# Kernel optimization log

Measured on AMD Instinct MI355X. Metric: run time of the kernel, lower is better.

## Reference

```python
import jax, jax.numpy as jnp
import numpy as np

MLOG32 = float(np.log(32.0))


def _maxpool(x, k):
    # F.max_pool2d(stride=1, padding=k//2) pads with -inf, matching init value
    pad = k // 2
    return jax.lax.reduce_window(x, -jnp.inf, jax.lax.max, (1, 1, k, k), (1, 1, 1, 1),
                                 ((0, 0), (0, 0), (pad, pad), (pad, pad)))


def _minpool(x, k):
    return -_maxpool(-x, k)


def _local_sum(x, k):
    # conv2d with all-ones kxk kernel, zero padding, same spatial size
    pad = k // 2
    return jax.lax.reduce_window(x, 0.0, jax.lax.add, (1, 1, k, k), (1, 1, 1, 1),
                                 ((0, 0), (0, 0), (pad, pad), (pad, pad)))


def _conv3(x, kern):
    # torch conv2d == cross-correlation == lax conv (no kernel flip)
    return jax.lax.conv_general_dilated(x, kern, (1, 1), ((1, 1), (1, 1)),
                                        dimension_numbers=('NCHW', 'OIHW', 'NCHW'))


def _otsu(gray, bins=32):
    # vectorized per-batch Otsu threshold; gray in [0,1]
    B, _, H, W = gray.shape
    v = gray.reshape(B, -1)
    idx = jnp.clip((v * bins).astype(jnp.int32), 0, bins - 1)  # histc semantics, v==1 -> last bin
    hist = jax.vmap(lambda i: jnp.bincount(i, length=bins))(idx).astype(gray.dtype)
    p = hist / (H * W + 1e-6)
    xs = jnp.linspace(0.0, 1.0, bins, dtype=gray.dtype)
    omega = jnp.cumsum(p, axis=1)
    mu = jnp.cumsum(p * xs[None, :], axis=1)
    mu_t = mu[:, -1:]
    sigma_b2 = (mu_t * omega - mu) ** 2 / (omega * (1.0 - omega) + 1e-8)
    kbest = jnp.argmax(sigma_b2, axis=1)
    edges = jnp.linspace(0.0, 1.0, bins + 1, dtype=gray.dtype)
    return edges[kbest].reshape(B, 1, 1, 1)


def _concept_maps(image_rgb, cell_dilate=10, k_local=9):
    r, g, b = image_rgb[:, 0:1], image_rgb[:, 1:2], image_rgb[:, 2:3]
    gray = jnp.clip(0.5 * (0.299 * r + 0.587 * g + 0.114 * b + 1.0), 0.0, 1.0)
    thr = _otsu(gray)
    nuc = (gray <= thr).astype(gray.dtype)
    # morphological open+close, k=3
    e = _minpool(nuc, 3)
    d = _maxpool(e, 3)
    d = _maxpool(d, 3)
    e2 = _minpool(d, 3)
    nuc = (e2 > 0.5).astype(gray.dtype)
    er = _minpool(nuc, 3)
    boundary = jnp.maximum(nuc - er, 0.0)
    lap_k = jnp.array([[0, 1, 0], [1, -4, 1], [0, 1, 0]], dtype=gray.dtype).reshape(1, 1, 3, 3)
    lap = jnp.abs(_conv3(nuc, lap_k))
    den = _local_sum(boundary, 5) + 1e-6
    roughness = lap * boundary / den
    kx = jnp.array([[1, 0, -1], [2, 0, -2], [1, 0, -1]], dtype=gray.dtype).reshape(1, 1, 3, 3)
    ky = jnp.array([[1, 2, 1], [0, 0, 0], [-1, -2, -1]], dtype=gray.dtype).reshape(1, 1, 3, 3)
    gx = _conv3(gray, kx)
    gy = _conv3(gray, ky)
    ang = jnp.arctan2(gy, gx)
    den_orient = _local_sum(jnp.ones_like(gray), k_local) + 1e-6
    ms = _local_sum(jnp.sin(ang), k_local) / den_orient
    mc = _local_sum(jnp.cos(ang), k_local) / den_orient
    circ_var = 1.0 - jnp.sqrt(ms ** 2 + mc ** 2 + 1e-6)
    kd = cell_dilate if cell_dilate % 2 == 1 else cell_dilate + 1  # force odd
    cell = jnp.minimum(_maxpool(nuc, kd), 1.0)
    A_n = _local_sum(nuc, k_local)
    A_c = jnp.maximum(_local_sum(cell, k_local) - A_n, 1.0)
    nc = A_n / A_c
    g2 = _local_sum(gray * gray, k_local) / den_orient
    g1 = _local_sum(gray, k_local) / den_orient
    ent_like = jnp.log1p(jnp.maximum(g2 - g1 * g1, 0.0))
    z_maps = jnp.concatenate([roughness, circ_var, nc, ent_like], axis=1)
    return z_maps, nuc


def _energy_forward(image_rgb, cal_a, cal_b, alpha_logits, tau_p, Ht, Wt):
    z_maps, nuc = _concept_maps(image_rgb)
    z0 = jnp.log1p(jnp.maximum(z_maps[:, 0:1], 0.0))
    z1 = jnp.clip(z_maps[:, 1:2], 0.0, 1.0)
    z2 = jnp.log1p(jnp.maximum(z_maps[:, 2:3], 0.0))
    z3 = jnp.clip(z_maps[:, 3:4], 0.0, MLOG32)
    z_stable = jnp.concatenate([z0, z1, z2, z3], axis=1)
    z_cal = jax.nn.softplus(cal_a)[None, :, None, None] * z_stable + cal_b[None, :, None, None]
    alpha = jax.nn.softmax(alpha_logits)[None, :, None, None]
    E = jnp.sum(alpha * z_cal, axis=1, keepdims=True)
    B = E.shape[0]
    if (E.shape[2], E.shape[3]) != (Ht, Wt):
        E_t = jax.image.resize(E, (B, 1, Ht, Wt), method='linear')
    else:
        E_t = E
    tau = 0.2 + jax.nn.softplus(tau_p)
    A = jax.nn.softmax((-E_t / tau).reshape(B, 1, Ht * Wt), axis=-1).reshape(B, 1, Ht, Wt)
    return A, z_maps, nuc, E_t


def setup_inputs() -> dict:
    key = jax.random.key(0)
    k1, k2, k3, k4 = jax.random.split(key, 4)
    B, H, W = 16, 512, 512
    image_rgb = 2.0 * jax.random.uniform(k1, (B, 3, H, W), dtype=jnp.float32) - 1.0
    cal_a = 1.0 + 0.1 * jax.random.normal(k2, (4,), jnp.float32)
    cal_b = 0.1 * jax.random.normal(k3, (4,), jnp.float32)
    alpha_logits = 0.1 * jax.random.normal(k4, (4,), jnp.float32)
    tau_p = jnp.float32(0.5)
    return {"image_rgb": image_rgb, "cal_a": cal_a, "cal_b": cal_b,
            "alpha_logits": alpha_logits, "tau_p": tau_p, "target_h": 512, "target_w": 512}


def reference(image_rgb, cal_a, cal_b, alpha_logits, tau_p, target_h, target_w):
    return _energy_forward(image_rgb, cal_a, cal_b, alpha_logits, tau_p, int(target_h), int(target_w))
```

## Files before the change

### kernel.cpp

```cpp
#include <hip/hip_runtime.h>
#include <math.h>
#include <stdint.h>

#define HW 512
#define IMG (HW*HW)
#define MLOG32f 3.4657359027997265f

__device__ __forceinline__ float grayf(float r, float g, float b) {
    float t = __fadd_rn(__fadd_rn(__fmul_rn(0.299f, r), __fmul_rn(0.587f, g)), __fmul_rn(0.114f, b));
    float s = __fmul_rn(0.5f, __fadd_rn(t, 1.0f));
    return fminf(fmaxf(s, 0.0f), 1.0f);
}

__device__ __forceinline__ float softplusf(float x) {
    return fmaxf(x, 0.0f) + log1pf(expf(-fabsf(x)));
}

__device__ __forceinline__ uint64_t kmask(int lo, int hi) {
    return (1ull << hi) - (1ull << lo);
}

__global__ void k_init(const float* __restrict__ cal_a, const float* __restrict__ cal_b,
                       const float* __restrict__ alpha_logits, const float* __restrict__ tau_p,
                       int* __restrict__ hist, float* __restrict__ expsum,
                       float* __restrict__ sc, int B) {
    int tid = threadIdx.x;
    for (int i = tid; i < B * 32; i += blockDim.x) hist[i] = 0;
    for (int i = tid; i < B; i += blockDim.x) expsum[i] = 0.0f;
    if (tid == 0) {
        float al[4];
        float m = -1e30f;
        for (int c = 0; c < 4; c++) { al[c] = alpha_logits[c]; m = fmaxf(m, al[c]); }
        float e[4]; float s = 0.0f;
        for (int c = 0; c < 4; c++) { e[c] = expf(al[c] - m); s += e[c]; }
        float bias = 0.0f;
        for (int c = 0; c < 4; c++) {
            float alpha = e[c] / s;
            sc[c] = alpha * softplusf(cal_a[c]);
            bias += alpha * cal_b[c];
        }
        sc[4] = bias;
        sc[5] = 0.2f + softplusf(tau_p[0]);
    }
}

__global__ __launch_bounds__(256) void k_gray_hist(const float* __restrict__ img,
                                                   float* __restrict__ gray,
                                                   int* __restrict__ hist) {
    __shared__ int lh[32];
    int tid = threadIdx.x;
    int b = blockIdx.y;
    if (tid < 32) lh[tid] = 0;
    __syncthreads();
    const float4* rp = (const float4*)(img + (size_t)b * 3 * IMG);
    const float4* gp = (const float4*)(img + (size_t)b * 3 * IMG + IMG);
    const float4* bp = (const float4*)(img + (size_t)b * 3 * IMG + 2 * IMG);
    float4* op = (float4*)(gray + (size_t)b * IMG);
    int i = blockIdx.x * 256 + tid;
    float4 r = rp[i], g = gp[i], bb = bp[i];
    float4 o;
    o.x = grayf(r.x, g.x, bb.x);
    o.y = grayf(r.y, g.y, bb.y);
    o.z = grayf(r.z, g.z, bb.z);
    o.w = grayf(r.w, g.w, bb.w);
    op[i] = o;
    int b0 = min(max((int)(o.x * 32.0f), 0), 31);
    int b1 = min(max((int)(o.y * 32.0f), 0), 31);
    int b2 = min(max((int)(o.z * 32.0f), 0), 31);
    int b3 = min(max((int)(o.w * 32.0f), 0), 31);
    atomicAdd(&lh[b0], 1); atomicAdd(&lh[b1], 1);
    atomicAdd(&lh[b2], 1); atomicAdd(&lh[b3], 1);
    __syncthreads();
    if (tid < 32) atomicAdd(&hist[b * 32 + tid], lh[tid]);
}

__global__ void k_otsu(const int* __restrict__ hist, float* __restrict__ thr, int B) {
    int b = threadIdx.x;
    if (b >= B) return;
    const int* h = hist + b * 32;
    float omega[32], mu[32];
    float co = 0.0f, cm = 0.0f;
    for (int k = 0; k < 32; k++) {
        float pk = (float)h[k] * (1.0f / 262144.0f);
        float xs = (float)((double)k / 31.0);
        co += pk;
        cm += pk * xs;
        omega[k] = co; mu[k] = cm;
    }
    float mu_t = mu[31];
    float best = -1e30f; int kb = 0;
    for (int k = 0; k < 32; k++) {
        float t = mu_t * omega[k] - mu[k];
        float sb = (t * t) / (omega[k] * (1.0f - omega[k]) + 1e-8f);
        if (sb > best) { best = sb; kb = k; }
    }
    thr[b] = (float)kb * 0.03125f;
}

__global__ __launch_bounds__(256) void k_thresh(const float* __restrict__ gray,
                                                const float* __restrict__ thr,
                                                uint32_t* __restrict__ packed) {
    int b = blockIdx.y;
    int i = blockIdx.x * 256 + threadIdx.x;
    float t = thr[b];
    float v = gray[(size_t)b * IMG + i];
    unsigned long long m = __ballot(v <= t);
    if ((threadIdx.x & 63) == 0)
        *(uint64_t*)&packed[(size_t)b * 8192 + (i >> 5)] = m;
}

__global__ __launch_bounds__(256) void k_morph(const uint32_t* __restrict__ p0,
                                               float* __restrict__ nuc,
                                               uint32_t* __restrict__ pn) {
    __shared__ uint64_t s0[40], s1[40];
    int tid = threadIdx.x, b = blockIdx.z;
    int x0 = blockIdx.x * 32, y0 = blockIdx.y * 32;
    int w0 = x0 >> 5;
    const uint32_t* pb = p0 + (size_t)b * 8192;
    int xlo = (x0 == 0) ? 4 : 0;
    int xhi = (x0 == 480) ? 36 : 40;
    uint64_t mwin = kmask(xlo, xhi);

    if (tid < 40) {
        int y = y0 - 4 + tid;
        uint64_t v = 0;
        if ((unsigned)y < (unsigned)HW) {
            const uint32_t* rowp = pb + y * 16;
            uint64_t wm = (w0 > 0)  ? rowp[w0 - 1] : 0;
            uint64_t wc = rowp[w0];
            uint64_t wp = (w0 < 15) ? rowp[w0 + 1] : 0;
            v = ((wm >> 28) | (wc << 4) | (wp << 36)) & kmask(0, 40);
        }
        s0[tid] = v;
    }
    __syncthreads();
    if (tid >= 1 && tid < 39) {
        uint64_t e = ~0ull;
        for (int dq = -1; dq <= 1; dq++) {
            int q = tid + dq;
            int y = y0 - 4 + q;
            uint64_t m = ((unsigned)y < (unsigned)HW) ? mwin : 0;
            uint64_t v = s0[q] | ~m;
            e &= v & (v << 1) & (v >> 1);
        }
        s1[tid] = e;
    }
    __syncthreads();
    if (tid >= 2 && tid < 38) {
        uint64_t d = 0;
        uint64_t me = kmask(1, 39);
        for (int dq = -1; dq <= 1; dq++) {
            int q = tid + dq;
            int y = y0 - 4 + q;
            uint64_t m = ((unsigned)y < (unsigned)HW) ? (mwin & me) : 0;
            uint64_t v = s1[q] & m;
            d |= v | (v << 1) | (v >> 1);
        }
        s0[tid] = d;
    }
    __syncthreads();
    if (tid >= 3 && tid < 37) {
        uint64_t d = 0;
        uint64_t me = kmask(2, 38);
        for (int dq = -1; dq <= 1; dq++) {
            int q = tid + dq;
            int y = y0 - 4 + q;
            uint64_t m = ((unsigned)y < (unsigned)HW) ? (mwin & me) : 0;
            uint64_t v = s0[q] & m;
            d |= v | (v << 1) | (v >> 1);
        }
        s1[tid] = d;
    }
    __syncthreads();
    if (tid >= 4 && tid < 36) {
        uint64_t e = ~0ull;
        uint64_t me = kmask(3, 37);
        for (int dq = -1; dq <= 1; dq++) {
            int q = tid + dq;
            int y = y0 - 4 + q;
            uint64_t m = ((unsigned)y < (unsigned)HW) ? (mwin & me) : 0;
            uint64_t v = s1[q] | ~m;
            e &= v & (v << 1) & (v >> 1);
        }
        s0[tid] = e;
    }
    __syncthreads();
    if (tid < 32) {
        int y = y0 + tid;
        pn[(size_t)b * 8192 + y * 16 + w0] = (uint32_t)(s0[tid + 4] >> 4);
    }
    float* nb = nuc + (size_t)b * IMG;
    for (int k = 0; k < 4; k++) {
        int i = tid + k * 256;
        int py = i >> 5, px = i & 31;
        nb[(size_t)(y0 + py) * HW + x0 + px] = (float)((s0[py + 4] >> (px + 4)) & 1);
    }
}

__global__ __launch_bounds__(256) void k_gray_maps(const float* __restrict__ gray,
                                                   float* zmap) {
    __shared__ float gt[42 * 43];
    __shared__ float st[40 * 41];
    __shared__ float ct[40 * 41];
    __shared__ float rs0[40 * 33];
    __shared__ float rs1[40 * 33];
    int tid = threadIdx.x, b = blockIdx.z;
    int x0 = blockIdx.x * 32, y0 = blockIdx.y * 32;
    const float* gb = gray + (size_t)b * IMG;
    for (int i = tid; i < 42 * 42; i += 256) {
        int ly = i / 42, lx = i % 42;
        int gy = y0 + ly - 5, gx = x0 + lx - 5;
        gt[ly * 43 + lx] = (gy >= 0 && gy < HW && gx >= 0 && gx < HW) ? gb[gy * HW + gx] : 0.0f;
    }
    __syncthreads();
    for (int i = tid; i < 1600; i += 256) {
        int ly = i / 40, lx = i % 40;
        int gy = y0 + ly - 4, gx = x0 + lx - 4;
        float s = 0.0f, c = 0.0f;
        if (gy >= 0 && gy < HW && gx >= 0 && gx < HW) {
            float a00 = gt[ly * 43 + lx],       a01 = gt[ly * 43 + lx + 1],       a02 = gt[ly * 43 + lx + 2];
            float a10 = gt[(ly + 1) * 43 + lx],                                   a12 = gt[(ly + 1) * 43 + lx + 2];
            float a20 = gt[(ly + 2) * 43 + lx], a21 = gt[(ly + 2) * 43 + lx + 1], a22 = gt[(ly + 2) * 43 + lx + 2];
            float gxv = (a00 - a02) + 2.0f * (a10 - a12) + (a20 - a22);
            float gyv = (a00 + 2.0f * a01 + a02) - (a20 + 2.0f * a21 + a22);
            float r2 = gxv * gxv + gyv * gyv;
            if (r2 > 0.0f) { float r = sqrtf(r2); s = gyv / r; c = gxv / r; }
            else { s = 0.0f; c = 1.0f; }
        }
        st[ly * 41 + lx] = s; ct[ly * 41 + lx] = c;
    }
    __syncthreads();
    for (int i = tid; i < 40 * 32; i += 256) {
        int ly = i / 32, lx = i % 32;
        float ss = 0.0f, cs = 0.0f;
        for (int dx = 0; dx < 9; dx++) { ss += st[ly * 41 + lx + dx]; cs += ct[ly * 41 + lx + dx]; }
        rs0[ly * 33 + lx] = ss; rs1[ly * 33 + lx] = cs;
    }
    __syncthreads();
    float z1v[4];
    for (int k = 0; k < 4; k++) {
        int j = tid + k * 256; int py = j >> 5, px = j & 31;
        float ss = 0.0f, cs = 0.0f;
        for (int dy = 0; dy < 9; dy++) { ss += rs0[(py + dy) * 33 + px]; cs += rs1[(py + dy) * 33 + px]; }
        int gy = y0 + py, gx = x0 + px;
        float cnty = (float)(min(gy + 4, HW - 1) - max(gy - 4, 0) + 1);
        float cntx = (float)(min(gx + 4, HW - 1) - max(gx - 4, 0) + 1);
        float den = cnty * cntx + 1e-6f;
        float ms = ss / den, mc = cs / den;
        z1v[k] = 1.0f - sqrtf(ms * ms + mc * mc + 1e-6f);
    }
    __syncthreads();
    for (int i = tid; i < 40 * 32; i += 256) {
        int ly = i / 32, lx = i % 32;
        float gs = 0.0f, g2s = 0.0f;
        for (int dx = 1; dx <= 9; dx++) { float v = gt[(ly + 1) * 43 + lx + dx]; gs += v; g2s += v * v; }
        rs0[ly * 33 + lx] = gs; rs1[ly * 33 + lx] = g2s;
    }
    __syncthreads();
    float* z1p = zmap + ((size_t)b * 4 + 1) * IMG;
    float* z3p = zmap + ((size_t)b * 4 + 3) * IMG;
    for (int k = 0; k < 4; k++) {
        int j = tid + k * 256; int py = j >> 5, px = j & 31;
        float gs = 0.0f, g2s = 0.0f;
        for (int dy = 0; dy < 9; dy++) { gs += rs0[(py + dy) * 33 + px]; g2s += rs1[(py + dy) * 33 + px]; }
        int gy = y0 + py, gx = x0 + px;
        float cnty = (float)(min(gy + 4, HW - 1) - max(gy - 4, 0) + 1);
        float cntx = (float)(min(gx + 4, HW - 1) - max(gx - 4, 0) + 1);
        float den = cnty * cntx + 1e-6f;
        float g1 = gs / den, g2 = g2s / den;
        z1p[gy * HW + gx] = z1v[k];
        z3p[gy * HW + gx] = log1pf(fmaxf(g2 - g1 * g1, 0.0f));
    }
}

__global__ __launch_bounds__(256) void k_nuc_maps(const uint32_t* __restrict__ pn,
                                                  float* zmap,
                                                  float* __restrict__ Eout,
                                                  const float* __restrict__ sc,
                                                  float* __restrict__ expsum) {
    __shared__ uint64_t nrow[50];
    __shared__ uint64_t ehr[50];
    __shared__ uint64_t dilh[50];
    __shared__ uint64_t bnd[36];
    __shared__ uint64_t cell[40];
    __shared__ int rs_n[40][32];
    __shared__ int rs_c[40][32];
    __shared__ int rs_b[36][32];
    __shared__ float red[256];
    int tid = threadIdx.x, b = blockIdx.z;
    int x0 = blockIdx.x * 32, y0 = blockIdx.y * 32;
    int w0 = x0 >> 5;
    const uint32_t* pb = pn + (size_t)b * 8192;
    int xlo = (x0 == 0) ? 9 : 0;
    int xhi = (x0 == 480) ? 41 : 50;
    uint64_t mwin = kmask(xlo, xhi);

    if (tid < 50) {
        int y = y0 - 9 + tid;
        uint64_t v = 0;
        if ((unsigned)y < (unsigned)HW) {
            const uint32_t* rowp = pb + y * 16;
            uint64_t wm = (w0 > 0)  ? rowp[w0 - 1] : 0;
            uint64_t wc = rowp[w0];
            uint64_t wp = (w0 < 15) ? rowp[w0 + 1] : 0;
            v = ((wm >> 23) | (wc << 9) | (wp << 41)) & kmask(0, 50);
        }
        nrow[tid] = v;
    }
    __syncthreads();
    if (tid < 50) {
        uint64_t v = nrow[tid];
        uint64_t d = v | (v << 1) | (v >> 1);
        d = d | (d << 2) | (d >> 2);
        d = d | (d << 2) | (d >> 2);
        dilh[tid] = d;
    }
    if (tid >= 6 && tid < 44) {
        int y = y0 - 9 + tid;
        uint64_t m = ((unsigned)y < (unsigned)HW) ? mwin : 0;
        uint64_t v = nrow[tid] | ~m;
        ehr[tid] = v & (v << 1) & (v >> 1);
    }
    __syncthreads();
    if (tid < 36) {
        int r = tid + 7;
        uint64_t er = ehr[r - 1] & ehr[r] & ehr[r + 1];
        bnd[tid] = nrow[r] & ~er;
    }
    if (tid < 40) {
        int r = tid + 5;
        int y = y0 - 4 + tid;
        uint64_t c = 0;
        for (int d = -5; d <= 5; d++) c |= dilh[r + d];
        uint64_t m = ((unsigned)y < (unsigned)HW) ? mwin : 0;
        cell[tid] = c & m;
    }
    __syncthreads();
    for (int i = tid; i < 40 * 32; i += 256) {
        int rr = i >> 5, p = i & 31;
        rs_n[rr][p] = __popcll((nrow[rr + 5] >> (p + 5)) & 0x1FFull);
        rs_c[rr][p] = __popcll((cell[rr]     >> (p + 5)) & 0x1FFull);
    }
    for (int i = tid; i < 36 * 32; i += 256) {
        int rr = i >> 5, p = i & 31;
        rs_b[rr][p] = __popcll((bnd[rr] >> (p + 7)) & 0x1Full);
    }
    __syncthreads();
    if (tid < 96) {
        int p = tid & 31, a = tid >> 5;
        if (a == 0)      { int s = 0; for (int rr = 0; rr < 40; rr++) { s += rs_n[rr][p]; rs_n[rr][p] = s; } }
        else if (a == 1) { int s = 0; for (int rr = 0; rr < 40; rr++) { s += rs_c[rr][p]; rs_c[rr][p] = s; } }
        else             { int s = 0; for (int rr = 0; rr < 36; rr++) { s += rs_b[rr][p]; rs_b[rr][p] = s; } }
    }
    __syncthreads();

    float w0f = sc[0], w1f = sc[1], w2f = sc[2], w3f = sc[3], bias = sc[4], tau = sc[5];
    const float* z1p = zmap + ((size_t)b * 4 + 1) * IMG;
    const float* z3p = zmap + ((size_t)b * 4 + 3) * IMG;
    float* z0p = zmap + ((size_t)b * 4 + 0) * IMG;
    float* z2p = zmap + ((size_t)b * 4 + 2) * IMG;
    float* Ep = Eout + (size_t)b * IMG;
    float acc = 0.0f;
    for (int k = 0; k < 4; k++) {
        int j = tid + k * 256; int py = j >> 5, p = j & 31;
        int An = rs_n[py + 8][p] - (py ? rs_n[py - 1][p] : 0);
        int Ac = rs_c[py + 8][p] - (py ? rs_c[py - 1][p] : 0);
        int db = rs_b[py + 4][p] - (py ? rs_b[py - 1][p] : 0);
        int r = py + 9, kk = p + 9;
        uint64_t rowc = nrow[r];
        int c   = (int)((rowc >> kk) & 1);
        int nb4 = (int)((nrow[r - 1] >> kk) & 1) + (int)((nrow[r + 1] >> kk) & 1)
                + (int)((rowc >> (kk - 1)) & 1) + (int)((rowc >> (kk + 1)) & 1);
        int lap = nb4 - 4 * c; lap = lap < 0 ? -lap : lap;
        int bc  = (int)((bnd[py + 2] >> kk) & 1);
        float den = (float)db + 1e-6f;
        float rough = (float)(lap * bc) / den;
        float z2 = (float)An / fmaxf((float)(Ac - An), 1.0f);
        int gy = y0 + py, gx = x0 + p;
        float z1 = z1p[gy * HW + gx], z3 = z3p[gy * HW + gx];
        float z0s = log1pf(fmaxf(rough, 0.0f));
        float z1s = fminf(fmaxf(z1, 0.0f), 1.0f);
        float z2s = log1pf(fmaxf(z2, 0.0f));
        float z3s = fminf(fmaxf(z3, 0.0f), MLOG32f);
        float E = w0f * z0s + w1f * z1s + w2f * z2s + w3f * z3s + bias;
        z0p[gy * HW + gx] = rough;
        z2p[gy * HW + gx] = z2;
        Ep[gy * HW + gx] = E;
        acc += expf(-E / tau);
    }
    red[tid] = acc;
    __syncthreads();
    for (int s = 128; s > 0; s >>= 1) {
        if (tid < s) red[tid] += red[tid + s];
        __syncthreads();
    }
    if (tid == 0) atomicAdd(&expsum[b], red[0]);
}

__global__ __launch_bounds__(256) void k_softmaxA(const float* __restrict__ E,
                                                  float* __restrict__ A,
                                                  const float* __restrict__ sc,
                                                  const float* __restrict__ expsum) {
    int b = blockIdx.y;
    int i = blockIdx.x * 256 + threadIdx.x;
    float tau = sc[5], S = expsum[b];
    const float4* Ep = (const float4*)(E + (size_t)b * IMG);
    float4* Ap = (float4*)(A + (size_t)b * IMG);
    float4 e = Ep[i];
    float4 o;
    o.x = expf(-e.x / tau) / S;
    o.y = expf(-e.y / tau) / S;
    o.z = expf(-e.z / tau) / S;
    o.w = expf(-e.w / tau) / S;
    Ap[i] = o;
}

extern "C" void kernel_launch(void* const* d_in, const int* in_sizes, int n_in,
                              void* d_out, int out_size, void* d_ws, size_t ws_size,
                              hipStream_t stream) {
    const float* img   = (const float*)d_in[0];
    const float* cal_a = (const float*)d_in[1];
    const float* cal_b = (const float*)d_in[2];
    const float* alpha = (const float*)d_in[3];
    const float* tau_p = (const float*)d_in[4];
    int B = in_sizes[0] / (3 * IMG);

    float* out  = (float*)d_out;
    float* A    = out;
    float* zmap = out + (size_t)B * IMG;
    float* nuc  = out + (size_t)B * IMG * 5;
    float* E    = out + (size_t)B * IMG * 6;
    float* gray = A;

    int*      hist    = (int*)d_ws;
    float*    thr     = (float*)d_ws + B * 32;
    float*    sc      = thr + B;
    float*    expsum  = sc + 8;
    uint32_t* packed0 = (uint32_t*)d_ws + 1024;
    uint32_t* packedN = packed0 + (size_t)B * 8192;

    k_init<<<1, 256, 0, stream>>>(cal_a, cal_b, alpha, tau_p, hist, expsum, sc, B);
    k_gray_hist<<<dim3(IMG / 1024, B), 256, 0, stream>>>(img, gray, hist);
    k_otsu<<<1, 64, 0, stream>>>(hist, thr, B);
    k_thresh<<<dim3(IMG / 256, B), 256, 0, stream>>>(gray, thr, packed0);
    dim3 tg(HW / 32, HW / 32, B);
    k_morph<<<tg, 256, 0, stream>>>(packed0, nuc, packedN);
    k_gray_maps<<<tg, 256, 0, stream>>>(gray, zmap);
    k_nuc_maps<<<tg, 256, 0, stream>>>(packedN, zmap, E, sc, expsum);
    k_softmaxA<<<dim3(IMG / 1024, B), 256, 0, stream>>>(E, A, sc, expsum);
}
```

Measured before the change: 287.6 us.

## Fuse gray-map and nucleus-map kernels, move nuc write, use fast math intrinsics

Merges k_gray_maps and k_nuc_maps into one k_maps kernel. The z1/z3 values stay in registers instead of being written to global memory and read back, and shared memory is aliased between the two phases. The float nuc map is now written from k_maps instead of k_morph. Divisions, sqrt, log1p and exp are replaced with hardware rcp/rsq/__logf/__expf, and the block reduction switches to wavefront shuffles. This trades some numerical precision for fewer instructions and less memory traffic.

Result: faster. 257.5 us (-10.5%).

```diff
diff --git a/kernel.cpp b/kernel.cpp
--- a/kernel.cpp
+++ b/kernel.cpp
@@ -15,6 +15,10 @@
 __device__ __forceinline__ float softplusf(float x) {
     return fmaxf(x, 0.0f) + log1pf(expf(-fabsf(x)));
 }
+
+__device__ __forceinline__ float frcp(float x)  { return __builtin_amdgcn_rcpf(x); }
+__device__ __forceinline__ float frsq(float x)  { return __builtin_amdgcn_rsqf(x); }
+__device__ __forceinline__ float flog1p(float x){ return __logf(1.0f + x); }
 
 __device__ __forceinline__ uint64_t kmask(int lo, int hi) {
     return (1ull << hi) - (1ull << lo);
@@ -40,7 +44,9 @@
             bias += alpha * cal_b[c];
         }
         sc[4] = bias;
-        sc[5] = 0.2f + softplusf(tau_p[0]);
+        float tau = 0.2f + softplusf(tau_p[0]);
+        sc[5] = tau;
+        sc[6] = -1.0f / tau;
     }
 }
 
@@ -110,7 +116,6 @@
 }
 
 __global__ __launch_bounds__(256) void k_morph(const uint32_t* __restrict__ p0,
-                                               float* __restrict__ nuc,
                                                uint32_t* __restrict__ pn) {
     __shared__ uint64_t s0[40], s1[40];
     int tid = threadIdx.x, b = blockIdx.z;
@@ -189,30 +194,68 @@
         int y = y0 + tid;
         pn[(size_t)b * 8192 + y * 16 + w0] = (uint32_t)(s0[tid + 4] >> 4);
     }
-    float* nb = nuc + (size_t)b * IMG;
-    for (int k = 0; k < 4; k++) {
-        int i = tid + k * 256;
-        int py = i >> 5, px = i & 31;
-        nb[(size_t)(y0 + py) * HW + x0 + px] = (float)((s0[py + 4] >> (px + 4)) & 1);
-    }
-}
-
-__global__ __launch_bounds__(256) void k_gray_maps(const float* __restrict__ gray,
-                                                   float* zmap) {
-    __shared__ float gt[42 * 43];
-    __shared__ float st[40 * 41];
-    __shared__ float ct[40 * 41];
-    __shared__ float rs0[40 * 33];
-    __shared__ float rs1[40 * 33];
+}
+
+__global__ __launch_bounds__(256) void k_maps(const float* __restrict__ gray,
+                                              const uint32_t* __restrict__ pn,
+                                              float* __restrict__ zmap,
+                                              float* __restrict__ nucf,
+                                              float* __restrict__ Eout,
+                                              const float* __restrict__ sc,
+                                              float* __restrict__ expsum) {
+    __shared__ __align__(16) char smem[30912];
+    __shared__ uint64_t nrow[50], ehr[50], dilh[50], bnd[36], cell[40];
+    __shared__ float red[4];
+    float* gt  = (float*)smem;
+    float* st  = (float*)(smem + 7232);
+    float* ct  = (float*)(smem + 13792);
+    float* rs0 = (float*)(smem + 20352);
+    float* rs1 = (float*)(smem + 25632);
+    int* rs_n = (int*)smem;
+    int* rs_c = (int*)(smem + 5120);
+    int* rs_b = (int*)(smem + 10240);
+
     int tid = threadIdx.x, b = blockIdx.z;
     int x0 = blockIdx.x * 32, y0 = blockIdx.y * 32;
+    int w0 = x0 >> 5;
     const float* gb = gray + (size_t)b * IMG;
+    const uint32_t* pb = pn + (size_t)b * 8192;
+    int xlo = (x0 == 0) ? 9 : 0;
+    int xhi = (x0 == 480) ? 41 : 50;
+    uint64_t mwin = kmask(xlo, xhi);
+
     for (int i = tid; i < 42 * 42; i += 256) {
         int ly = i / 42, lx = i % 42;
         int gy = y0 + ly - 5, gx = x0 + lx - 5;
         gt[ly * 43 + lx] = (gy >= 0 && gy < HW && gx >= 0 && gx < HW) ? gb[gy * HW + gx] : 0.0f;
     }
-    __syncthreads();
+    if (tid < 50) {
+        int y = y0 - 9 + tid;
+        uint64_t v = 0;
+        if ((unsigned)y < (unsigned)HW) {
+            const uint32_t* rowp = pb + y * 16;
+            uint64_t wm = (w0 > 0)  ? rowp[w0 - 1] : 0;
+            uint64_t wc = rowp[w0];
+            uint64_t wp = (w0 < 15) ? rowp[w0 + 1] : 0;
+            v = ((wm >> 23) | (wc << 9) | (wp << 41)) & kmask(0, 50);
+        }
+        nrow[tid] = v;
+    }
+    __syncthreads();
+
+    if (tid < 50) {
+        uint64_t v = nrow[tid];
+        uint64_t d = v | (v << 1) | (v >> 1);
+        d = d | (d << 2) | (d >> 2);
+        d = d | (d << 2) | (d >> 2);
+        dilh[tid] = d;
+    }
+    if (tid >= 6 && tid < 44) {
+        int y = y0 - 9 + tid;
+        uint64_t m = ((unsigned)y < (unsigned)HW) ? mwin : 0;
+        uint64_t v = nrow[tid] | ~m;
+        ehr[tid] = v & (v << 1) & (v >> 1);
+    }
     for (int i = tid; i < 1600; i += 256) {
         int ly = i / 40, lx = i % 40;
         int gy = y0 + ly - 4, gx = x0 + lx - 4;
@@ -224,19 +267,34 @@
             float gxv = (a00 - a02) + 2.0f * (a10 - a12) + (a20 - a22);
             float gyv = (a00 + 2.0f * a01 + a02) - (a20 + 2.0f * a21 + a22);
             float r2 = gxv * gxv + gyv * gyv;
-            if (r2 > 0.0f) { float r = sqrtf(r2); s = gyv / r; c = gxv / r; }
+            if (r2 > 0.0f) { float ir = frsq(r2); s = gyv * ir; c = gxv * ir; }
             else { s = 0.0f; c = 1.0f; }
         }
         st[ly * 41 + lx] = s; ct[ly * 41 + lx] = c;
     }
     __syncthreads();
+
+    if (tid < 36) {
+        int r = tid + 7;
+        uint64_t er = ehr[r - 1] & ehr[r] & ehr[r + 1];
+        bnd[tid] = nrow[r] & ~er;
+    }
+    if (tid < 40) {
+        int r = tid + 5;
+        int y = y0 - 4 + tid;
+        uint64_t c = 0;
+        for (int d = -5; d <= 5; d++) c |= dilh[r + d];
+        uint64_t m = ((unsigned)y < (unsigned)HW) ? mwin : 0;
+        cell[tid] = c & m;
+    }
     for (int i = tid; i < 40 * 32; i += 256) {
-        int ly = i / 32, lx = i % 32;
+        int ly = i >> 5, lx = i & 31;
         float ss = 0.0f, cs = 0.0f;
         for (int dx = 0; dx < 9; dx++) { ss += st[ly * 41 + lx + dx]; cs += ct[ly * 41 + lx + dx]; }
         rs0[ly * 33 + lx] = ss; rs1[ly * 33 + lx] = cs;
     }
     __syncthreads();
+
     float z1v[4];
     for (int k = 0; k < 4; k++) {
         int j = tid + k * 256; int py = j >> 5, px = j & 31;
@@ -245,20 +303,19 @@
         int gy = y0 + py, gx = x0 + px;
         float cnty = (float)(min(gy + 4, HW - 1) - max(gy - 4, 0) + 1);
         float cntx = (float)(min(gx + 4, HW - 1) - max(gx - 4, 0) + 1);
-        float den = cnty * cntx + 1e-6f;
-        float ms = ss / den, mc = cs / den;
+        float iden = frcp(cnty * cntx + 1e-6f);
+        float ms = ss * iden, mc = cs * iden;
         z1v[k] = 1.0f - sqrtf(ms * ms + mc * mc + 1e-6f);
     }
     __syncthreads();
     for (int i = tid; i < 40 * 32; i += 256) {
-        int ly = i / 32, lx = i % 32;
+        int ly = i >> 5, lx = i & 31;
         float gs = 0.0f, g2s = 0.0f;
         for (int dx = 1; dx <= 9; dx++) { float v = gt[(ly + 1) * 43 + lx + dx]; gs += v; g2s += v * v; }
         rs0[ly * 33 + lx] = gs; rs1[ly * 33 + lx] = g2s;
     }
     __syncthreads();
-    float* z1p = zmap + ((size_t)b * 4 + 1) * IMG;
-    float* z3p = zmap + ((size_t)b * 4 + 3) * IMG;
+    float z3v[4];
     for (int k = 0; k < 4; k++) {
         int j = tid + k * 256; int py = j >> 5, px = j & 31;
         float gs = 0.0f, g2s = 0.0f;
@@ -266,135 +323,71 @@
         int gy = y0 + py, gx = x0 + px;
         float cnty = (float)(min(gy + 4, HW - 1) - max(gy - 4, 0) + 1);
         float cntx = (float)(min(gx + 4, HW - 1) - max(gx - 4, 0) + 1);
-        float den = cnty * cntx + 1e-6f;
-        float g1 = gs / den, g2 = g2s / den;
-        z1p[gy * HW + gx] = z1v[k];
-        z3p[gy * HW + gx] = log1pf(fmaxf(g2 - g1 * g1, 0.0f));
-    }
-}
-
-__global__ __launch_bounds__(256) void k_nuc_maps(const uint32_t* __restrict__ pn,
-                                                  float* zmap,
-                                                  float* __restrict__ Eout,
-                                                  const float* __restrict__ sc,
-                                                  float* __restrict__ expsum) {
-    __shared__ uint64_t nrow[50];
-    __shared__ uint64_t ehr[50];
-    __shared__ uint64_t dilh[50];
-    __shared__ uint64_t bnd[36];
-    __shared__ uint64_t cell[40];
-    __shared__ int rs_n[40][32];
-    __shared__ int rs_c[40][32];
-    __shared__ int rs_b[36][32];
-    __shared__ float red[256];
-    int tid = threadIdx.x, b = blockIdx.z;
-    int x0 = blockIdx.x * 32, y0 = blockIdx.y * 32;
-    int w0 = x0 >> 5;
-    const uint32_t* pb = pn + (size_t)b * 8192;
-    int xlo = (x0 == 0) ? 9 : 0;
-    int xhi = (x0 == 480) ? 41 : 50;
-    uint64_t mwin = kmask(xlo, xhi);
-
-    if (tid < 50) {
-        int y = y0 - 9 + tid;
-        uint64_t v = 0;
-        if ((unsigned)y < (unsigned)HW) {
-            const uint32_t* rowp = pb + y * 16;
-            uint64_t wm = (w0 > 0)  ? rowp[w0 - 1] : 0;
-            uint64_t wc = rowp[w0];
-            uint64_t wp = (w0 < 15) ? rowp[w0 + 1] : 0;
-            v = ((wm >> 23) | (wc << 9) | (wp << 41)) & kmask(0, 50);
-        }
-        nrow[tid] = v;
-    }
-    __syncthreads();
-    if (tid < 50) {
-        uint64_t v = nrow[tid];
-        uint64_t d = v | (v << 1) | (v >> 1);
-        d = d | (d << 2) | (d >> 2);
-        d = d | (d << 2) | (d >> 2);
-        dilh[tid] = d;
-    }
-    if (tid >= 6 && tid < 44) {
-        int y = y0 - 9 + tid;
-        uint64_t m = ((unsigned)y < (unsigned)HW) ? mwin : 0;
-        uint64_t v = nrow[tid] | ~m;
-        ehr[tid] = v & (v << 1) & (v >> 1);
-    }
-    __syncthreads();
-    if (tid < 36) {
-        int r = tid + 7;
-        uint64_t er = ehr[r - 1] & ehr[r] & ehr[r + 1];
-        bnd[tid] = nrow[r] & ~er;
-    }
-    if (tid < 40) {
-        int r = tid + 5;
-        int y = y0 - 4 + tid;
-        uint64_t c = 0;
-        for (int d = -5; d <= 5; d++) c |= dilh[r + d];
-        uint64_t m = ((unsigned)y < (unsigned)HW) ? mwin : 0;
-        cell[tid] = c & m;
-    }
-    __syncthreads();
+        float iden = frcp(cnty * cntx + 1e-6f);
+        float g1 = gs * iden, g2 = g2s * iden;
+        z3v[k] = flog1p(fmaxf(g2 - g1 * g1, 0.0f));
+    }
+    __syncthreads();
+
     for (int i = tid; i < 40 * 32; i += 256) {
         int rr = i >> 5, p = i & 31;
-        rs_n[rr][p] = __popcll((nrow[rr + 5] >> (p + 5)) & 0x1FFull);
-        rs_c[rr][p] = __popcll((cell[rr]     >> (p + 5)) & 0x1FFull);
+        rs_n[rr * 32 + p] = __popcll((nrow[rr + 5] >> (p + 5)) & 0x1FFull);
+        rs_c[rr * 32 + p] = __popcll((cell[rr]     >> (p + 5)) & 0x1FFull);
     }
     for (int i = tid; i < 36 * 32; i += 256) {
         int rr = i >> 5, p = i & 31;
-        rs_b[rr][p] = __popcll((bnd[rr] >> (p + 7)) & 0x1Full);
+        rs_b[rr * 32 + p] = __popcll((bnd[rr] >> (p + 7)) & 0x1Full);
     }
     __syncthreads();
     if (tid < 96) {
         int p = tid & 31, a = tid >> 5;
-        if (a == 0)      { int s = 0; for (int rr = 0; rr < 40; rr++) { s += rs_n[rr][p]; rs_n[rr][p] = s; } }
-        else if (a == 1) { int s = 0; for (int rr = 0; rr < 40; rr++) { s += rs_c[rr][p]; rs_c[rr][p] = s; } }
-        else             { int s = 0; for (int rr = 0; rr < 36; rr++) { s += rs_b[rr][p]; rs_b[rr][p] = s; } }
-    }
-    __syncthreads();
-
-    float w0f = sc[0], w1f = sc[1], w2f = sc[2], w3f = sc[3], bias = sc[4], tau = sc[5];
-    const float* z1p = zmap + ((size_t)b * 4 + 1) * IMG;
-    const float* z3p = zmap + ((size_t)b * 4 + 3) * IMG;
+        if (a == 0)      { int s = 0; for (int rr = 0; rr < 40; rr++) { s += rs_n[rr * 32 + p]; rs_n[rr * 32 + p] = s; } }
+        else if (a == 1) { int s = 0; for (int rr = 0; rr < 40; rr++) { s += rs_c[rr * 32 + p]; rs_c[rr * 32 + p] = s; } }
+        else             { int s = 0; for (int rr = 0; rr < 36; rr++) { s += rs_b[rr * 32 + p]; rs_b[rr * 32 + p] = s; } }
+    }
+    __syncthreads();
+
+    float w0f = sc[0], w1f = sc[1], w2f = sc[2], w3f = sc[3], bias = sc[4], ntau = sc[6];
     float* z0p = zmap + ((size_t)b * 4 + 0) * IMG;
+    float* z1p = zmap + ((size_t)b * 4 + 1) * IMG;
     float* z2p = zmap + ((size_t)b * 4 + 2) * IMG;
-    float* Ep = Eout + (size_t)b * IMG;
+    float* z3p = zmap + ((size_t)b * 4 + 3) * IMG;
+    float* Ep  = Eout + (size_t)b * IMG;
+    float* np  = nucf + (size_t)b * IMG;
     float acc = 0.0f;
     for (int k = 0; k < 4; k++) {
         int j = tid + k * 256; int py = j >> 5, p = j & 31;
-        int An = rs_n[py + 8][p] - (py ? rs_n[py - 1][p] : 0);
-        int Ac = rs_c[py + 8][p] - (py ? rs_c[py - 1][p] : 0);
-        int db = rs_b[py + 4][p] - (py ? rs_b[py - 1][p] : 0);
+        int An = rs_n[(py + 8) * 32 + p] - (py ? rs_n[(py - 1) * 32 + p] : 0);
+        int Ac = rs_c[(py + 8) * 32 + p] - (py ? rs_c[(py - 1) * 32 + p] : 0);
+        int db = rs_b[(py + 4) * 32 + p] - (py ? rs_b[(py - 1) * 32 + p] : 0);
         int r = py + 9, kk = p + 9;
         uint64_t rowc = nrow[r];
-        int c   = (int)((rowc >> kk) & 1);
-        int nb4 = (int)((nrow[r - 1] >> kk) & 1) + (int)((nrow[r + 1] >> kk) & 1)
-                + (int)((rowc >> (kk - 1)) & 1) + (int)((rowc >> (kk + 1)) & 1);
-        int lap = nb4 - 4 * c; lap = lap < 0 ? -lap : lap;
+        int cbit = (int)((rowc >> kk) & 1);
+        int nb4  = (int)((nrow[r - 1] >> kk) & 1) + (int)((nrow[r + 1] >> kk) & 1)
+                 + (int)((rowc >> (kk - 1)) & 1) + (int)((rowc >> (kk + 1)) & 1);
+        int lap = nb4 - 4 * cbit; lap = lap < 0 ? -lap : lap;
         int bc  = (int)((bnd[py + 2] >> kk) & 1);
-        float den = (float)db + 1e-6f;
-        float rough = (float)(lap * bc) / den;
-        float z2 = (float)An / fmaxf((float)(Ac - An), 1.0f);
+        float rough = (float)(lap * bc) * frcp((float)db + 1e-6f);
+        float z2 = (float)An * frcp(fmaxf((float)(Ac - An), 1.0f));
+        float z0s = flog1p(fmaxf(rough, 0.0f));
+        float z1s = fminf(fmaxf(z1v[k], 0.0f), 1.0f);
+        float z2s = flog1p(fmaxf(z2, 0.0f));
+        float z3s = fminf(fmaxf(z3v[k], 0.0f), MLOG32f);
+        float E = w0f * z0s + w1f * z1s + w2f * z2s + w3f * z3s + bias;
         int gy = y0 + py, gx = x0 + p;
-        float z1 = z1p[gy * HW + gx], z3 = z3p[gy * HW + gx];
-        float z0s = log1pf(fmaxf(rough, 0.0f));
-        float z1s = fminf(fmaxf(z1, 0.0f), 1.0f);
-        float z2s = log1pf(fmaxf(z2, 0.0f));
-        float z3s = fminf(fmaxf(z3, 0.0f), MLOG32f);
-        float E = w0f * z0s + w1f * z1s + w2f * z2s + w3f * z3s + bias;
-        z0p[gy * HW + gx] = rough;
-        z2p[gy * HW + gx] = z2;
-        Ep[gy * HW + gx] = E;
-        acc += expf(-E / tau);
-    }
-    red[tid] = acc;
-    __syncthreads();
-    for (int s = 128; s > 0; s >>= 1) {
-        if (tid < s) red[tid] += red[tid + s];
-        __syncthreads();
-    }
-    if (tid == 0) atomicAdd(&expsum[b], red[0]);
+        size_t o = (size_t)gy * HW + gx;
+        z0p[o] = rough;
+        z1p[o] = z1v[k];
+        z2p[o] = z2;
+        z3p[o] = z3v[k];
+        Ep[o]  = E;
+        np[o]  = (float)cbit;
+        acc += __expf(E * ntau);
+    }
+    for (int off = 32; off > 0; off >>= 1) acc += __shfl_down(acc, off, 64);
+    if ((tid & 63) == 0) red[tid >> 6] = acc;
+    __syncthreads();
+    if (tid == 0) atomicAdd(&expsum[b], red[0] + red[1] + red[2] + red[3]);
 }
 
 __global__ __launch_bounds__(256) void k_softmaxA(const float* __restrict__ E,
@@ -403,15 +396,16 @@
                                                   const float* __restrict__ expsum) {
     int b = blockIdx.y;
     int i = blockIdx.x * 256 + threadIdx.x;
-    float tau = sc[5], S = expsum[b];
+    float ntau = sc[6];
+    float invS = 1.0f / expsum[b];
     const float4* Ep = (const float4*)(E + (size_t)b * IMG);
     float4* Ap = (float4*)(A + (size_t)b * IMG);
     float4 e = Ep[i];
     float4 o;
-    o.x = expf(-e.x / tau) / S;
-    o.y = expf(-e.y / tau) / S;
-    o.z = expf(-e.z / tau) / S;
-    o.w = expf(-e.w / tau) / S;
+    o.x = __expf(e.x * ntau) * invS;
+    o.y = __expf(e.y * ntau) * invS;
+    o.z = __expf(e.z * ntau) * invS;
+    o.w = __expf(e.w * ntau) * invS;
     Ap[i] = o;
 }
 
@@ -444,8 +438,7 @@
     k_otsu<<<1, 64, 0, stream>>>(hist, thr, B);
     k_thresh<<<dim3(IMG / 256, B), 256, 0, stream>>>(gray, thr, packed0);
     dim3 tg(HW / 32, HW / 32, B);
-    k_morph<<<tg, 256, 0, stream>>>(packed0, nuc, packedN);
-    k_gray_maps<<<tg, 256, 0, stream>>>(gray, zmap);
-    k_nuc_maps<<<tg, 256, 0, stream>>>(packedN, zmap, E, sc, expsum);
+    k_morph<<<tg, 256, 0, stream>>>(packed0, packedN);
+    k_maps<<<tg, 256, 0, stream>>>(gray, packedN, zmap, nuc, E, sc, expsum);
     k_softmaxA<<<dim3(IMG / 1024, B), 256, 0, stream>>>(E, A, sc, expsum);
 }
```
